# Kernel optimization log

Hardware: AMD Instinct MI355X
Metric: run time of the kernel (lower is better)

The kernel has to match this reference:

```python
import jax, jax.numpy as jnp
import numpy as np

B, N, C, H, R = 16, 1024, 768, 12, 16
HD = C // H
SCALE = HD ** -0.5


def setup_inputs() -> dict:
    key = jax.random.key(0)
    ks = jax.random.split(key, 13)
    f = lambda k, shape, s=0.02: jax.random.normal(k, shape, dtype=jnp.float32) * s
    return {
        "x": jax.random.normal(ks[0], (B, N, C), dtype=jnp.float32),
        "W_qkv": f(ks[1], (3 * C, C)),
        "b_qkv": f(ks[2], (3 * C,)),
        "W_proj": f(ks[3], (C, C)),
        "b_proj": f(ks[4], (C,)),
        "A_q": f(ks[5], (R, C)),
        "B_q": f(ks[6], (C, R)),
        "A_k": f(ks[7], (R, C)),
        "B_k": f(ks[8], (C, R)),
        "A_v": f(ks[9], (R, C)),
        "B_v": f(ks[10], (C, R)),
        "A_o": f(ks[11], (R, C)),
        "B_o": f(ks[12], (C, R)),
    }


def _lora(x, A, Bu):
    # Adapter with no norm/act/bias, scaling=1.0: low-rank x @ A^T @ B^T
    return (x @ A.T) @ Bu.T


def _heads(t):
    # [B, N, C] -> [B, H, N, HD]
    return t.reshape(B, N, H, HD).transpose(0, 2, 1, 3)


def reference(x, W_qkv, b_qkv, W_proj, b_proj, A_q, B_q, A_k, B_k, A_v, B_v, A_o, B_o):
    qkv = x @ W_qkv.T + b_qkv                    # [B, N, 3C]
    qkv = qkv.reshape(B, N, 3, H, HD).transpose(2, 0, 3, 1, 4)  # [3, B, H, N, HD]
    q, k, v = qkv[0], qkv[1], qkv[2]
    q = q + _heads(_lora(x, A_q, B_q))
    k = k + _heads(_lora(x, A_k, B_k))
    v = v + _heads(_lora(x, A_v, B_v))
    attn = jnp.einsum("bhnd,bhmd->bhnm", q, k) * SCALE
    attn = jax.nn.softmax(attn, axis=-1)
    out = jnp.einsum("bhnm,bhmd->bhnd", attn, v)  # [B, H, N, HD]
    out = out.transpose(0, 2, 1, 3).reshape(B, N, C)
    out = out @ W_proj.T + b_proj
    out = out + _lora(out, A_o, B_o)
    return out
```

## Files before the change

kernel.cpp:

```cpp
#include <hip/hip_runtime.h>
#include <cmath>


#define DEVI __device__ __forceinline__

typedef float f32x4 __attribute__((ext_vector_type(4)));
typedef short s16x8 __attribute__((ext_vector_type(8)));
typedef __bf16 b16x8 __attribute__((ext_vector_type(8)));
typedef unsigned int u32x4 __attribute__((ext_vector_type(4)));

static constexpr int MTOT = 16384;
static constexpr int C = 768;
static constexpr int N3 = 2304;

DEVI unsigned short f2bf(float x) {
  unsigned int u = __builtin_bit_cast(unsigned int, x);
  return (unsigned short)((u + 0x7FFFu + ((u >> 16) & 1u)) >> 16);
}

DEVI f32x4 mfma16(s16x8 a, s16x8 b, f32x4 c) {
  return __builtin_amdgcn_mfma_f32_16x16x32_bf16(
      __builtin_bit_cast(b16x8, a), __builtin_bit_cast(b16x8, b), c, 0, 0, 0);
}

DEVI void async16(const void* g, void* l) {
  __builtin_amdgcn_global_load_lds(
      (__attribute__((address_space(1))) void*)g,
      (__attribute__((address_space(3))) void*)l, 16, 0, 0);
}


__global__ __launch_bounds__(256) void k_prep_x(const float* __restrict__ x,
                                                unsigned short* __restrict__ xb) {
  int idx = (blockIdx.x * 256 + threadIdx.x) * 4;
  float4 v = *(const float4*)(x + idx);
  uint2 p;
  p.x = (unsigned int)f2bf(v.x) | ((unsigned int)f2bf(v.y) << 16);
  p.y = (unsigned int)f2bf(v.z) | ((unsigned int)f2bf(v.w) << 16);
  *(uint2*)(xb + idx) = p;
}

__global__ __launch_bounds__(256) void k_prep_wqkv(
    const float* __restrict__ W, const float* __restrict__ Aq,
    const float* __restrict__ Bq, const float* __restrict__ Ak,
    const float* __restrict__ Bk, const float* __restrict__ Av,
    const float* __restrict__ Bv, unsigned short* __restrict__ out) {
  int idx = blockIdx.x * 256 + threadIdx.x;
  int n = idx / 768, c = idx - n * 768;
  int s = n / 768, co = n - s * 768;
  const float* A = (s == 0) ? Aq : (s == 1) ? Ak : Av;
  const float* Bm = (s == 0) ? Bq : (s == 1) ? Bk : Bv;
  float acc = W[idx];
#pragma unroll
  for (int r = 0; r < 16; ++r) acc += Bm[co * 16 + r] * A[r * 768 + c];
  out[idx] = f2bf(acc);
}

__global__ __launch_bounds__(256) void k_prep_M(const float* __restrict__ Ao,
                                                const float* __restrict__ Wp,
                                                float* __restrict__ M) {
  int r = blockIdx.x, t = threadIdx.x;
  float a0 = 0.f, a1 = 0.f, a2 = 0.f;
  for (int c = 0; c < 768; ++c) {
    float a = Ao[r * 768 + c];
    a0 += a * Wp[c * 768 + t];
    a1 += a * Wp[c * 768 + t + 256];
    a2 += a * Wp[c * 768 + t + 512];
  }
  M[r * 768 + t] = a0;
  M[r * 768 + t + 256] = a1;
  M[r * 768 + t + 512] = a2;
}

__global__ __launch_bounds__(256) void k_prep_wpe(const float* __restrict__ Wp,
                                                  const float* __restrict__ Bo,
                                                  const float* __restrict__ M,
                                                  unsigned short* __restrict__ out) {
  int idx = blockIdx.x * 256 + threadIdx.x;
  int n = idx / 768, j = idx - n * 768;
  float acc = Wp[idx];
#pragma unroll
  for (int r = 0; r < 16; ++r) acc += Bo[n * 16 + r] * M[r * 768 + j];
  out[idx] = f2bf(acc);
}

__global__ __launch_bounds__(256) void k_prep_beff(const float* __restrict__ bp,
                                                   const float* __restrict__ Ao,
                                                   const float* __restrict__ Bo,
                                                   float* __restrict__ beff) {
  __shared__ float bv[16];
  int t = threadIdx.x;
  if (t < 16) {
    float a0 = 0.f, a1 = 0.f, a2 = 0.f;
    for (int c = 0; c < 256; ++c) {
      a0 += Ao[t * 768 + c] * bp[c];
      a1 += Ao[t * 768 + c + 256] * bp[c + 256];
      a2 += Ao[t * 768 + c + 512] * bp[c + 512];
    }
    bv[t] = a0 + a1 + a2;
  }
  __syncthreads();
  int n = blockIdx.x * 256 + t;
  float acc = bp[n];
#pragma unroll
  for (int r = 0; r < 16; ++r) acc += Bo[n * 16 + r] * bv[r];
  beff[n] = acc;
}


__global__ __launch_bounds__(256) void k_gemm_qkv(
    const unsigned short* __restrict__ A, const unsigned short* __restrict__ Bw,
    const float* __restrict__ bias, unsigned short* __restrict__ qb,
    unsigned short* __restrict__ kb, unsigned short* __restrict__ vtb) {
  __shared__ short la[128 * 32];
  __shared__ short lb[128 * 32];
  const int t = threadIdx.x;
  const int w = t >> 6, l = t & 63;
  const int i = l & 15, qd = l >> 4;
  const int wm = w >> 1, wn = w & 1;
  const int mblk = blockIdx.x, nblk = blockIdx.y;

  const unsigned short* Ab = A + (size_t)(mblk * 128) * 768;
  const unsigned short* Bb = Bw + (size_t)(nblk * 128) * 768;
  const int sr = l >> 2;
  const int sc = (l & 3) * 8;

  f32x4 acc[4][4] = {};

  for (int kb_ = 0; kb_ < 24; ++kb_) {
    const int k0 = kb_ * 32;
#pragma unroll
    for (int j = 0; j < 2; ++j) {
      const int row = w * 32 + j * 16 + sr;
      async16(Ab + row * 768 + k0 + sc, &la[(w * 32 + j * 16) * 32]);
      async16(Bb + row * 768 + k0 + sc, &lb[(w * 32 + j * 16) * 32]);
    }
    __syncthreads();
    s16x8 af[4], bf[4];
#pragma unroll
    for (int mi = 0; mi < 4; ++mi)
      af[mi] = *(const s16x8*)&la[(wm * 64 + mi * 16 + i) * 32 + qd * 8];
#pragma unroll
    for (int ni = 0; ni < 4; ++ni)
      bf[ni] = *(const s16x8*)&lb[(wn * 64 + ni * 16 + i) * 32 + qd * 8];
#pragma unroll
    for (int mi = 0; mi < 4; ++mi)
#pragma unroll
      for (int ni = 0; ni < 4; ++ni)
        acc[mi][ni] = mfma16(af[mi], bf[ni], acc[mi][ni]);
    __syncthreads();
  }

  const float c1 = 0.18033688011112042f;
#pragma unroll
  for (int ni = 0; ni < 4; ++ni) {
    const int n = nblk * 128 + wn * 64 + ni * 16 + i;
    const int s = n / 768;
    const int nrel = n - s * 768;
    const int h = nrel >> 6, d = nrel & 63;
    const float bvv = bias[n];
    if (s == 2) {
#pragma unroll
      for (int mi = 0; mi < 4; ++mi) {
        const int m0 = mblk * 128 + wm * 64 + mi * 16 + qd * 4;
        const int b = m0 >> 10, pos0 = m0 & 1023;
        uint2 pk;
        pk.x = (unsigned int)f2bf(acc[mi][ni][0] + bvv) |
               ((unsigned int)f2bf(acc[mi][ni][1] + bvv) << 16);
        pk.y = (unsigned int)f2bf(acc[mi][ni][2] + bvv) |
               ((unsigned int)f2bf(acc[mi][ni][3] + bvv) << 16);
        *(uint2*)&vtb[(size_t)((b * 12 + h) * 64 + d) * 1024 + pos0] = pk;
      }
    } else {
      unsigned short* dst = (s == 0) ? qb : kb;
      const float scl = (s == 0) ? c1 : 1.0f;
#pragma unroll
      for (int mi = 0; mi < 4; ++mi) {
#pragma unroll
        for (int r = 0; r < 4; ++r) {
          const int m = mblk * 128 + wm * 64 + mi * 16 + qd * 4 + r;
          const int b = m >> 10, pos = m & 1023;
          dst[(size_t)((b * 12 + h) * 1024 + pos) * 64 + d] =
              f2bf((acc[mi][ni][r] + bvv) * scl);
        }
      }
    }
  }
}


__global__ __launch_bounds__(256, 4) void k_attn(
    const unsigned short* __restrict__ qg, const unsigned short* __restrict__ kg,
    const unsigned short* __restrict__ vtg, unsigned short* __restrict__ og) {
  __shared__ short k_lds[2][64 * 64];
  __shared__ short vt_lds[2][64 * 64];

  const int t = threadIdx.x;
  const int w = t >> 6, l = t & 63;
  const int i = l & 15, qd = l >> 4;
  const int ix7 = l & 7;
  const int bh = blockIdx.x;
  const int qblk = blockIdx.y;
  const int h = bh % 12, b = bh / 12;

  const unsigned short* Qg = qg + (size_t)(bh * 1024 + qblk * 128) * 64;
  const unsigned short* Kg = kg + (size_t)bh * 1024 * 64;
  const unsigned short* Vtg = vtg + (size_t)bh * 64 * 1024;

  const int srl = l >> 3;
  const int sgc = (l & 7) ^ srl;

  s16x8 qf[2][2];
#pragma unroll
  for (int nq = 0; nq < 2; ++nq)
#pragma unroll
    for (int k0 = 0; k0 < 2; ++k0)
      qf[nq][k0] =
          *(const s16x8*)(Qg + (w * 32 + nq * 16 + i) * 64 + k0 * 32 + qd * 8);

  auto stage = [&](int bufn, int tkv) {
#pragma unroll
    for (int it = 0; it < 2; ++it) {
      const int rbase = it * 32 + w * 8;
      async16(Kg + (size_t)(tkv * 64 + rbase + srl) * 64 + sgc * 8,
              &k_lds[bufn][rbase * 64]);
      async16(Vtg + (size_t)(rbase + srl) * 1024 + tkv * 64 + sgc * 8,
              &vt_lds[bufn][rbase * 64]);
    }
  };

  stage(0, 0);

  f32x4 oacc[2][4] = {};
  f32x4 lacc[2] = {};
  const u32x4 ones_u = {0x3F803F80u, 0x3F803F80u, 0u, 0u};
  const s16x8 ones = __builtin_bit_cast(s16x8, ones_u);

  for (int tkv = 0; tkv < 16; ++tkv) {
    const int buf = tkv & 1;
    __syncthreads();
    if (tkv < 15) stage(buf ^ 1, tkv + 1);

#pragma unroll
    for (int mi = 0; mi < 4; ++mi) {
      f32x4 st[2] = {};
#pragma unroll
      for (int k0 = 0; k0 < 2; ++k0) {
        const s16x8 kf = *(const s16x8*)&k_lds[buf][(mi * 16 + i) * 64 +
                                                    (((k0 * 4 + qd) ^ ix7) * 8)];
        st[0] = mfma16(kf, qf[0][k0], st[0]);
        st[1] = mfma16(kf, qf[1][k0], st[1]);
      }

      s16x8 pa[2];
#pragma unroll
      for (int mq = 0; mq < 2; ++mq) {
        unsigned int u0 = __builtin_bit_cast(
            unsigned int, __builtin_amdgcn_exp2f(st[mq][0]));
        unsigned int u1 = __builtin_bit_cast(
            unsigned int, __builtin_amdgcn_exp2f(st[mq][1]));
        unsigned int u2 = __builtin_bit_cast(
            unsigned int, __builtin_amdgcn_exp2f(st[mq][2]));
        unsigned int u3 = __builtin_bit_cast(
            unsigned int, __builtin_amdgcn_exp2f(st[mq][3]));
        u32x4 p;
        p[0] = __builtin_amdgcn_perm(u1, u0, 0x07060302u);
        p[1] = __builtin_amdgcn_perm(u3, u2, 0x07060302u);
        p[2] = 0u;
        p[3] = 0u;
        pa[mq] = __builtin_bit_cast(s16x8, p);
      }

#pragma unroll
      for (int nd = 0; nd < 4; ++nd) {
        const uint2 v = *(const uint2*)&vt_lds[buf][(nd * 16 + i) * 64 +
                                                    ((((mi * 2 + (qd >> 1)) ^ ix7) * 8) +
                                                     (qd & 1) * 4)];
        u32x4 vu = {v.x, v.y, 0u, 0u};
        const s16x8 vf = __builtin_bit_cast(s16x8, vu);
        oacc[0][nd] = mfma16(pa[0], vf, oacc[0][nd]);
        oacc[1][nd] = mfma16(pa[1], vf, oacc[1][nd]);
      }
      lacc[0] = mfma16(pa[0], ones, lacc[0]);
      lacc[1] = mfma16(pa[1], ones, lacc[1]);
    }
  }

  const int orow0 = qblk * 128 + w * 32;
#pragma unroll
  for (int mq = 0; mq < 2; ++mq) {
    float linv[4];
#pragma unroll
    for (int r = 0; r < 4; ++r) linv[r] = 1.0f / lacc[mq][r];
#pragma unroll
    for (int nd = 0; nd < 4; ++nd)
#pragma unroll
      for (int r = 0; r < 4; ++r) {
        const int pos = orow0 + mq * 16 + qd * 4 + r;
        const int d = nd * 16 + i;
        og[(size_t)(b * 1024 + pos) * 768 + h * 64 + d] =
            f2bf(oacc[mq][nd][r] * linv[r]);
      }
  }
}


__global__ __launch_bounds__(256) void k_gemm_proj(
    const unsigned short* __restrict__ A, const unsigned short* __restrict__ Bw,
    const float* __restrict__ bias, float* __restrict__ out) {
  __shared__ short la[128 * 32];
  __shared__ short lb[128 * 32];
  const int t = threadIdx.x;
  const int w = t >> 6, l = t & 63;
  const int i = l & 15, qd = l >> 4;
  const int wm = w >> 1, wn = w & 1;
  const int mblk = blockIdx.x, nblk = blockIdx.y;

  const unsigned short* Ab = A + (size_t)(mblk * 128) * 768;
  const unsigned short* Bb = Bw + (size_t)(nblk * 128) * 768;
  const int sr = l >> 2;
  const int sc = (l & 3) * 8;

  f32x4 acc[4][4] = {};

  for (int kb_ = 0; kb_ < 24; ++kb_) {
    const int k0 = kb_ * 32;
#pragma unroll
    for (int j = 0; j < 2; ++j) {
      const int row = w * 32 + j * 16 + sr;
      async16(Ab + row * 768 + k0 + sc, &la[(w * 32 + j * 16) * 32]);
      async16(Bb + row * 768 + k0 + sc, &lb[(w * 32 + j * 16) * 32]);
    }
    __syncthreads();
    s16x8 af[4], bf[4];
#pragma unroll
    for (int mi = 0; mi < 4; ++mi)
      af[mi] = *(const s16x8*)&la[(wm * 64 + mi * 16 + i) * 32 + qd * 8];
#pragma unroll
    for (int ni = 0; ni < 4; ++ni)
      bf[ni] = *(const s16x8*)&lb[(wn * 64 + ni * 16 + i) * 32 + qd * 8];
#pragma unroll
    for (int mi = 0; mi < 4; ++mi)
#pragma unroll
      for (int ni = 0; ni < 4; ++ni)
        acc[mi][ni] = mfma16(af[mi], bf[ni], acc[mi][ni]);
    __syncthreads();
  }

#pragma unroll
  for (int ni = 0; ni < 4; ++ni) {
    const int n = nblk * 128 + wn * 64 + ni * 16 + i;
    const float bvv = bias[n];
#pragma unroll
    for (int mi = 0; mi < 4; ++mi) {
#pragma unroll
      for (int r = 0; r < 4; ++r) {
        const int m = mblk * 128 + wm * 64 + mi * 16 + qd * 4 + r;
        out[(size_t)m * 768 + n] = acc[mi][ni][r] + bvv;
      }
    }
  }
}


extern "C" void kernel_launch(void* const* d_in, const int* in_sizes, int n_in,
                              void* d_out, int out_size, void* d_ws, size_t ws_size,
                              hipStream_t stream) {
  const float* x = (const float*)d_in[0];
  const float* Wqkv = (const float*)d_in[1];
  const float* bqkv = (const float*)d_in[2];
  const float* Wp = (const float*)d_in[3];
  const float* bp = (const float*)d_in[4];
  const float* Aq = (const float*)d_in[5];
  const float* Bq = (const float*)d_in[6];
  const float* Ak = (const float*)d_in[7];
  const float* Bk = (const float*)d_in[8];
  const float* Av = (const float*)d_in[9];
  const float* Bv = (const float*)d_in[10];
  const float* Ao = (const float*)d_in[11];
  const float* Bo = (const float*)d_in[12];
  float* out = (float*)d_out;

  unsigned short* xb = (unsigned short*)d_ws;
  unsigned short* wqkvb = xb + (size_t)MTOT * C;
  unsigned short* wpeb = wqkvb + (size_t)N3 * C;
  unsigned short* qb = wpeb + (size_t)C * C;
  unsigned short* kb = qb + (size_t)MTOT * C;
  unsigned short* vtb = kb + (size_t)MTOT * C;
  float* Mbuf = (float*)(vtb + (size_t)MTOT * C);
  float* beff = Mbuf + 16 * 768;
  unsigned short* ob = xb;

  k_prep_x<<<12288, 256, 0, stream>>>(x, xb);
  k_prep_wqkv<<<6912, 256, 0, stream>>>(Wqkv, Aq, Bq, Ak, Bk, Av, Bv, wqkvb);
  k_prep_M<<<16, 256, 0, stream>>>(Ao, Wp, Mbuf);
  k_prep_wpe<<<2304, 256, 0, stream>>>(Wp, Bo, Mbuf, wpeb);
  k_prep_beff<<<3, 256, 0, stream>>>(bp, Ao, Bo, beff);

  k_gemm_qkv<<<dim3(128, 18), 256, 0, stream>>>(xb, wqkvb, bqkv, qb, kb, vtb);
  k_attn<<<dim3(192, 8), 256, 0, stream>>>(qb, kb, vtb, ob);
  k_gemm_proj<<<dim3(128, 6), 256, 0, stream>>>(ob, wpeb, beff, out);
}
```

Baseline: 400.2 us.

## Double-buffer GEMM LDS tiles and swap MFMA operands for vectorized epilogue stores

Both the QKV and projection GEMMs now use two LDS buffers, so the async load of the next K-slice is issued while MFMAs run on the current one, and one barrier per iteration is dropped. The MFMA operands are swapped so each lane holds four consecutive output columns. This lets the Q/K and projection epilogues write packed uint2/float4 stores with a float4 bias load instead of scalar strided stores. The QKV GEMM is split into two template launches: a swapped one for Q/K and the original layout for the transposed V. The cost is double the LDS per block, which may lower occupancy, plus one extra kernel launch.

After: 415.5 us. 1.04x slower.

```diff
diff --git a/kernel.cpp b/kernel.cpp
--- a/kernel.cpp
+++ b/kernel.cpp
@@ -108,58 +108,90 @@
 }
 
 
-__global__ __launch_bounds__(256) void k_gemm_qkv(
+template <bool SWAP>
+__global__ __launch_bounds__(256) void k_gemm_qkv_t(
     const unsigned short* __restrict__ A, const unsigned short* __restrict__ Bw,
-    const float* __restrict__ bias, unsigned short* __restrict__ qb,
+    const float* __restrict__ bias, int nblk0, unsigned short* __restrict__ qb,
     unsigned short* __restrict__ kb, unsigned short* __restrict__ vtb) {
-  __shared__ short la[128 * 32];
-  __shared__ short lb[128 * 32];
+  __shared__ short la[2][128 * 32];
+  __shared__ short lb[2][128 * 32];
   const int t = threadIdx.x;
   const int w = t >> 6, l = t & 63;
   const int i = l & 15, qd = l >> 4;
   const int wm = w >> 1, wn = w & 1;
-  const int mblk = blockIdx.x, nblk = blockIdx.y;
+  const int mblk = blockIdx.x, nblk = nblk0 + blockIdx.y;
 
   const unsigned short* Ab = A + (size_t)(mblk * 128) * 768;
   const unsigned short* Bb = Bw + (size_t)(nblk * 128) * 768;
   const int sr = l >> 2;
   const int sc = (l & 3) * 8;
 
-  f32x4 acc[4][4] = {};
-
-  for (int kb_ = 0; kb_ < 24; ++kb_) {
+  auto stage = [&](int bufn, int kb_) {
     const int k0 = kb_ * 32;
 #pragma unroll
     for (int j = 0; j < 2; ++j) {
       const int row = w * 32 + j * 16 + sr;
-      async16(Ab + row * 768 + k0 + sc, &la[(w * 32 + j * 16) * 32]);
-      async16(Bb + row * 768 + k0 + sc, &lb[(w * 32 + j * 16) * 32]);
-    }
+      async16(Ab + row * 768 + k0 + sc, &la[bufn][(w * 32 + j * 16) * 32]);
+      async16(Bb + row * 768 + k0 + sc, &lb[bufn][(w * 32 + j * 16) * 32]);
+    }
+  };
+
+  stage(0, 0);
+
+  f32x4 acc[4][4] = {};
+
+  for (int kb_ = 0; kb_ < 24; ++kb_) {
+    const int buf = kb_ & 1;
     __syncthreads();
+    if (kb_ < 23) stage(buf ^ 1, kb_ + 1);
     s16x8 af[4], bf[4];
 #pragma unroll
     for (int mi = 0; mi < 4; ++mi)
-      af[mi] = *(const s16x8*)&la[(wm * 64 + mi * 16 + i) * 32 + qd * 8];
+      af[mi] = *(const s16x8*)&la[buf][(wm * 64 + mi * 16 + i) * 32 + qd * 8];
 #pragma unroll
     for (int ni = 0; ni < 4; ++ni)
-      bf[ni] = *(const s16x8*)&lb[(wn * 64 + ni * 16 + i) * 32 + qd * 8];
+      bf[ni] = *(const s16x8*)&lb[buf][(wn * 64 + ni * 16 + i) * 32 + qd * 8];
 #pragma unroll
     for (int mi = 0; mi < 4; ++mi)
 #pragma unroll
-      for (int ni = 0; ni < 4; ++ni)
-        acc[mi][ni] = mfma16(af[mi], bf[ni], acc[mi][ni]);
-    __syncthreads();
+      for (int ni = 0; ni < 4; ++ni) {
+        if constexpr (SWAP)
+          acc[mi][ni] = mfma16(bf[ni], af[mi], acc[mi][ni]);
+        else
+          acc[mi][ni] = mfma16(af[mi], bf[ni], acc[mi][ni]);
+      }
   }
 
   const float c1 = 0.18033688011112042f;
-#pragma unroll
-  for (int ni = 0; ni < 4; ++ni) {
-    const int n = nblk * 128 + wn * 64 + ni * 16 + i;
-    const int s = n / 768;
-    const int nrel = n - s * 768;
-    const int h = nrel >> 6, d = nrel & 63;
-    const float bvv = bias[n];
-    if (s == 2) {
+  if constexpr (SWAP) {
+#pragma unroll
+    for (int ni = 0; ni < 4; ++ni) {
+      const int n0 = nblk * 128 + wn * 64 + ni * 16 + qd * 4;
+      const int s = n0 / 768;
+      const int nrel = n0 - s * 768;
+      const int h = nrel >> 6, d0 = nrel & 63;
+      const float4 bv4 = *(const float4*)(bias + n0);
+      unsigned short* dst = (s == 0) ? qb : kb;
+      const float scl = (s == 0) ? c1 : 1.0f;
+#pragma unroll
+      for (int mi = 0; mi < 4; ++mi) {
+        const int m = mblk * 128 + wm * 64 + mi * 16 + i;
+        const int b = m >> 10, pos = m & 1023;
+        uint2 pk;
+        pk.x = (unsigned int)f2bf((acc[mi][ni][0] + bv4.x) * scl) |
+               ((unsigned int)f2bf((acc[mi][ni][1] + bv4.y) * scl) << 16);
+        pk.y = (unsigned int)f2bf((acc[mi][ni][2] + bv4.z) * scl) |
+               ((unsigned int)f2bf((acc[mi][ni][3] + bv4.w) * scl) << 16);
+        *(uint2*)&dst[(size_t)((b * 12 + h) * 1024 + pos) * 64 + d0] = pk;
+      }
+    }
+  } else {
+#pragma unroll
+    for (int ni = 0; ni < 4; ++ni) {
+      const int n = nblk * 128 + wn * 64 + ni * 16 + i;
+      const int nrel = n - 1536;
+      const int h = nrel >> 6, d = nrel & 63;
+      const float bvv = bias[n];
 #pragma unroll
       for (int mi = 0; mi < 4; ++mi) {
         const int m0 = mblk * 128 + wm * 64 + mi * 16 + qd * 4;
@@ -170,19 +202,6 @@
         pk.y = (unsigned int)f2bf(acc[mi][ni][2] + bvv) |
                ((unsigned int)f2bf(acc[mi][ni][3] + bvv) << 16);
         *(uint2*)&vtb[(size_t)((b * 12 + h) * 64 + d) * 1024 + pos0] = pk;
-      }
-    } else {
-      unsigned short* dst = (s == 0) ? qb : kb;
-      const float scl = (s == 0) ? c1 : 1.0f;
-#pragma unroll
-      for (int mi = 0; mi < 4; ++mi) {
-#pragma unroll
-        for (int r = 0; r < 4; ++r) {
-          const int m = mblk * 128 + wm * 64 + mi * 16 + qd * 4 + r;
-          const int b = m >> 10, pos = m & 1023;
-          dst[(size_t)((b * 12 + h) * 1024 + pos) * 64 + d] =
-              f2bf((acc[mi][ni][r] + bvv) * scl);
-        }
       }
     }
   }
@@ -308,8 +327,8 @@
 __global__ __launch_bounds__(256) void k_gemm_proj(
     const unsigned short* __restrict__ A, const unsigned short* __restrict__ Bw,
     const float* __restrict__ bias, float* __restrict__ out) {
-  __shared__ short la[128 * 32];
-  __shared__ short lb[128 * 32];
+  __shared__ short la[2][128 * 32];
+  __shared__ short lb[2][128 * 32];
   const int t = threadIdx.x;
   const int w = t >> 6, l = t & 63;
   const int i = l & 15, qd = l >> 4;
@@ -321,43 +340,51 @@
   const int sr = l >> 2;
   const int sc = (l & 3) * 8;
 
-  f32x4 acc[4][4] = {};
-
-  for (int kb_ = 0; kb_ < 24; ++kb_) {
+  auto stage = [&](int bufn, int kb_) {
     const int k0 = kb_ * 32;
 #pragma unroll
     for (int j = 0; j < 2; ++j) {
       const int row = w * 32 + j * 16 + sr;
-      async16(Ab + row * 768 + k0 + sc, &la[(w * 32 + j * 16) * 32]);
-      async16(Bb + row * 768 + k0 + sc, &lb[(w * 32 + j * 16) * 32]);
-    }
+      async16(Ab + row * 768 + k0 + sc, &la[bufn][(w * 32 + j * 16) * 32]);
+      async16(Bb + row * 768 + k0 + sc, &lb[bufn][(w * 32 + j * 16) * 32]);
+    }
+  };
+
+  stage(0, 0);
+
+  f32x4 acc[4][4] = {};
+
+  for (int kb_ = 0; kb_ < 24; ++kb_) {
+    const int buf = kb_ & 1;
     __syncthreads();
+    if (kb_ < 23) stage(buf ^ 1, kb_ + 1);
     s16x8 af[4], bf[4];
 #pragma unroll
     for (int mi = 0; mi < 4; ++mi)
-      af[mi] = *(const s16x8*)&la[(wm * 64 + mi * 16 + i) * 32 + qd * 8];
+      af[mi] = *(const s16x8*)&la[buf][(wm * 64 + mi * 16 + i) * 32 + qd * 8];
 #pragma unroll
     for (int ni = 0; ni < 4; ++ni)
-      bf[ni] = *(const s16x8*)&lb[(wn * 64 + ni * 16 + i) * 32 + qd * 8];
+      bf[ni] = *(const s16x8*)&lb[buf][(wn * 64 + ni * 16 + i) * 32 + qd * 8];
 #pragma unroll
     for (int mi = 0; mi < 4; ++mi)
 #pragma unroll
       for (int ni = 0; ni < 4; ++ni)
-        acc[mi][ni] = mfma16(af[mi], bf[ni], acc[mi][ni]);
-    __syncthreads();
+        acc[mi][ni] = mfma16(bf[ni], af[mi], acc[mi][ni]);
   }
 
 #pragma unroll
   for (int ni = 0; ni < 4; ++ni) {
-    const int n = nblk * 128 + wn * 64 + ni * 16 + i;
-    const float bvv = bias[n];
+    const int n0 = nblk * 128 + wn * 64 + ni * 16 + qd * 4;
+    const float4 bv4 = *(const float4*)(bias + n0);
 #pragma unroll
     for (int mi = 0; mi < 4; ++mi) {
-#pragma unroll
-      for (int r = 0; r < 4; ++r) {
-        const int m = mblk * 128 + wm * 64 + mi * 16 + qd * 4 + r;
-        out[(size_t)m * 768 + n] = acc[mi][ni][r] + bvv;
-      }
+      const int m = mblk * 128 + wm * 64 + mi * 16 + i;
+      float4 o;
+      o.x = acc[mi][ni][0] + bv4.x;
+      o.y = acc[mi][ni][1] + bv4.y;
+      o.z = acc[mi][ni][2] + bv4.z;
+      o.w = acc[mi][ni][3] + bv4.w;
+      *(float4*)&out[(size_t)m * 768 + n0] = o;
     }
   }
 }
@@ -397,7 +424,10 @@
   k_prep_wpe<<<2304, 256, 0, stream>>>(Wp, Bo, Mbuf, wpeb);
   k_prep_beff<<<3, 256, 0, stream>>>(bp, Ao, Bo, beff);
 
-  k_gemm_qkv<<<dim3(128, 18), 256, 0, stream>>>(xb, wqkvb, bqkv, qb, kb, vtb);
+  k_gemm_qkv_t<true><<<dim3(128, 12), 256, 0, stream>>>(xb, wqkvb, bqkv, 0,
+                                                        qb, kb, vtb);
+  k_gemm_qkv_t<false><<<dim3(128, 6), 256, 0, stream>>>(xb, wqkvb, bqkv, 12,
+                                                        qb, kb, vtb);
   k_attn<<<dim3(192, 8), 256, 0, stream>>>(qb, kb, vtb, ob);
   k_gemm_proj<<<dim3(128, 6), 256, 0, stream>>>(ob, wpeb, beff, out);
 }
```
